# Kernel tuning notes

Hardware: AMD Instinct MI355X
Metric: run time of the kernel (lower is better)

Reference implementation:

```python
import jax, jax.numpy as jnp
import numpy as np

B, S, D, H = 4, 2048, 1024, 16
DK = D // H
SCALE = 1.0 / np.float32(np.sqrt(DK))


def setup_inputs() -> dict:
    key = jax.random.key(0)
    ks = jax.random.split(key, 11)
    w = lambda k: (jax.random.normal(k, (D, D), jnp.float32) * 0.02)
    b = lambda k: (jax.random.normal(k, (D,), jnp.float32) * 0.02)
    return {
        "Q": jax.random.normal(ks[0], (B, S, D), jnp.float32),
        "K": jax.random.normal(ks[1], (B, S, D), jnp.float32),
        "V": jax.random.normal(ks[2], (B, S, D), jnp.float32),
        "Wq": w(ks[3]), "bq": b(ks[4]),
        "Wk": w(ks[5]), "bk": b(ks[6]),
        "Wv": w(ks[7]), "bv": b(ks[8]),
        "Wo": w(ks[9]), "bo": b(ks[10]),
        # causal mask, broadcast over batch and heads: [1,1,S,S]
        "mask": jnp.tril(jnp.ones((1, 1, S, S), dtype=bool)),
    }


def reference(Q, K, V, Wq, bq, Wk, bk, Wv, bv, Wo, bo, mask):
    def proj(x, W, bias):
        # [B,S,D] -> [B,H,S,DK]
        return (x @ W + bias).reshape(B, S, H, DK).transpose(0, 2, 1, 3)

    q = proj(Q, Wq, bq)
    k = proj(K, Wk, bk)
    v = proj(V, Wv, bv)
    scores = jnp.einsum("bhqd,bhkd->bhqk", q, k) * SCALE  # [B,H,S,S]
    scores = jnp.where(mask, scores, jnp.float32(-1e9))
    attn = jax.nn.softmax(scores, axis=-1)
    out = jnp.einsum("bhqk,bhkd->bhqd", attn, v)  # [B,H,S,DK]
    out = out.transpose(0, 2, 1, 3).reshape(B, S, D)
    return out @ Wo + bo
```

## Files before the change

### kernel.cpp

```cpp
#include <hip/hip_runtime.h>
#include <hip/hip_bf16.h>
#include <stdint.h>

#define BB 4
#define SS 2048
#define DD 1024
#define HH 16
#define DKK 64
#define MM (BB * SS)

typedef __hip_bfloat16 bf16;
typedef __attribute__((ext_vector_type(8))) short frag8;
typedef __attribute__((ext_vector_type(4))) float f32x4;

#define GLDS16(g, l)                                                        \
  __builtin_amdgcn_global_load_lds(                                         \
      (const __attribute__((address_space(1))) void*)(g),                   \
      (__attribute__((address_space(3))) void*)(l), 16, 0, 0)

#define MFMA __builtin_amdgcn_mfma_f32_16x16x32_bf16
#define SBAR asm volatile("s_barrier" ::: "memory")
#define WAITV0 asm volatile("s_waitcnt vmcnt(0)" ::: "memory")

__device__ __forceinline__ unsigned short f2bu(float f) {
  __hip_bfloat16 h = __float2bfloat16(f);
  return *reinterpret_cast<unsigned short*>(&h);
}

struct WtArgs {
  const float* s[3];
  unsigned short* d[3];
};
__global__ __launch_bounds__(256) void wtrans_kernel(WtArgs a) {
  const float* __restrict__ W = a.s[blockIdx.z];
  unsigned short* __restrict__ Wt = a.d[blockIdx.z];
  __shared__ float t[64][68];
  const int n0 = blockIdx.x * 64, k0 = blockIdx.y * 64;
  const int tid = threadIdx.x;
#pragma unroll
  for (int it = 0; it < 4; ++it) {
    const int kk = it * 16 + (tid >> 4);
    const int nn = (tid & 15) * 4;
    const float4 v = *(const float4*)&W[(size_t)(k0 + kk) * DD + n0 + nn];
    *(float4*)&t[kk][nn] = v;
  }
  __syncthreads();
#pragma unroll
  for (int it = 0; it < 2; ++it) {
    const int n = it * 32 + (tid >> 3);
    const int c = tid & 7;
    frag8 pk;
#pragma unroll
    for (int j = 0; j < 8; ++j) pk[j] = (short)f2bu(t[c * 8 + j][n]);
    *(frag8*)&Wt[(size_t)(n0 + n) * DD + k0 + c * 8] = pk;
  }
}

struct CvtArgs {
  const float* s[3];
  unsigned short* d[3];
};
__global__ __launch_bounds__(256) void cvt_kernel(CvtArgs a) {
  const float* __restrict__ src = a.s[blockIdx.y];
  unsigned short* __restrict__ dst = a.d[blockIdx.y];
  const size_t i = ((size_t)blockIdx.x * 256 + threadIdx.x) * 8;
  const float4 v0 = *(const float4*)&src[i];
  const float4 v1 = *(const float4*)&src[i + 4];
  frag8 pk;
  pk[0] = (short)f2bu(v0.x); pk[1] = (short)f2bu(v0.y);
  pk[2] = (short)f2bu(v0.z); pk[3] = (short)f2bu(v0.w);
  pk[4] = (short)f2bu(v1.x); pk[5] = (short)f2bu(v1.y);
  pk[6] = (short)f2bu(v1.z); pk[7] = (short)f2bu(v1.w);
  *(frag8*)&dst[i] = pk;
}

struct GArgs {
  const void* A[3];
  const unsigned short* W[3];
  const float* bias[3];
  void* out[3];
  float oscale[3];
  int abf16[3];
  int omode[3];
};

__global__ __launch_bounds__(512, 2) void gemm8_kernel(GArgs ga) {
  constexpr int K = DD;
  const int nwg = gridDim.x;
  const int q = nwg >> 3;
  const int o = blockIdx.x;
  const int wgid = (o & 7) * q + (o >> 3);
  const int z = wgid >> 7;
  const int rem = wgid & 127;
  const int mt = rem >> 2, nt = rem & 3;
  const int m0 = mt * 256, n0 = nt * 256;

  const unsigned short* __restrict__ A = (const unsigned short*)ga.A[z];
  const unsigned short* __restrict__ Wt = ga.W[z];
  const float* __restrict__ bias = ga.bias[z];
  void* __restrict__ outv = ga.out[z];
  const float oscale = ga.oscale[z];
  const int omode = ga.omode[z];

  __shared__ unsigned short As[2][256 * 64];
  __shared__ unsigned short Bs[2][256 * 64];

  const int tid = threadIdx.x;
  const int wave = tid >> 6, lane = tid & 63, quad = lane >> 4, l15 = lane & 15;
  const int wr = wave >> 2, wc = wave & 3;

  f32x4 acc[8][4] = {};
  frag8 af[4][2], bfv[2][2];

  auto stage4 = [&](int b, int k0, int half) {
#pragma unroll
    for (int ii = 0; ii < 4; ++ii) {
      const int i = half * 4 + ii;
      const int g = i * 8 + wave;
      const int rs = (g & 31) * 8;
      const int lrow = rs + (lane >> 3);
      const int gc = ((lane & 7) ^ (lane >> 3)) * 8;
      const unsigned off = __builtin_amdgcn_readfirstlane(
          (unsigned)(b * 32768 + rs * 128));
      if (g < 32) {
        GLDS16(&A[(size_t)(m0 + lrow) * K + k0 + gc], (char*)&As[0][0] + off);
      } else {
        GLDS16(&Wt[(size_t)(n0 + lrow) * K + k0 + gc], (char*)&Bs[0][0] + off);
      }
    }
  };
  auto rdA = [&](int bt, int mh) {
#pragma unroll
    for (int mi = 0; mi < 4; ++mi)
#pragma unroll
      for (int s = 0; s < 2; ++s)
        af[mi][s] = *(const frag8*)&As[bt][(wr * 128 + mh * 64 + mi * 16 + l15) *
                                              64 +
                                          (((s * 4 + quad) ^ (l15 & 7)) * 8)];
  };
  auto rdB = [&](int bt, int nh) {
#pragma unroll
    for (int ni = 0; ni < 2; ++ni)
#pragma unroll
      for (int s = 0; s < 2; ++s)
        bfv[ni][s] = *(const frag8*)&Bs[bt][(wc * 64 + nh * 32 + ni * 16 + l15) *
                                                64 +
                                            (((s * 4 + quad) ^ (l15 & 7)) * 8)];
  };
  auto mma = [&](int mh, int nh) {
    __builtin_amdgcn_s_setprio(1);
#pragma unroll
    for (int s = 0; s < 2; ++s)
#pragma unroll
      for (int mi = 0; mi < 4; ++mi)
#pragma unroll
        for (int ni = 0; ni < 2; ++ni)
          acc[mh * 4 + mi][nh * 2 + ni] = MFMA(
              af[mi][s], bfv[ni][s], acc[mh * 4 + mi][nh * 2 + ni], 0, 0, 0);
    __builtin_amdgcn_s_setprio(0);
  };

  stage4(0, 0, 0);
  stage4(0, 0, 1);
  WAITV0;
  __syncthreads();

#pragma unroll 1
  for (int t = 0; t < 16; ++t) {
    const int bt = t & 1;
    const int nb = bt ^ 1;
    const bool pf = (t + 1 < 16);
    const int k1 = (t + 1) * 64;
    if (pf) stage4(nb, k1, 0);
    rdA(bt, 0);
    rdB(bt, 0);
    SBAR;
    mma(0, 0);
    SBAR;
    if (pf) stage4(nb, k1, 1);
    rdB(bt, 1);
    SBAR;
    mma(0, 1);
    SBAR;
    rdA(bt, 1);
    rdB(bt, 0);
    SBAR;
    mma(1, 0);
    SBAR;
    rdB(bt, 1);
    SBAR;
    mma(1, 1);
    WAITV0;
    SBAR;
  }

#pragma unroll
  for (int mi = 0; mi < 8; ++mi) {
#pragma unroll
    for (int ni = 0; ni < 4; ++ni) {
#pragma unroll
      for (int r = 0; r < 4; ++r) {
        const int grow = m0 + wr * 128 + mi * 16 + quad * 4 + r;
        const int gcol = n0 + wc * 64 + ni * 16 + l15;
        const float val = (acc[mi][ni][r] + bias[gcol]) * oscale;
        if (omode == 2) {
          ((float*)outv)[(size_t)grow * DD + gcol] = val;
        } else {
          const int b = grow / SS, s = grow % SS;
          const int h = gcol / DKK, dk = gcol % DKK;
          unsigned short* outp = (unsigned short*)outv;
          if (omode == 0)
            outp[(((size_t)(b * HH + h)) * SS + s) * DKK + dk] = f2bu(val);
          else
            outp[(((size_t)(b * HH + h)) * DKK + dk) * SS + s] = f2bu(val);
        }
      }
    }
  }
}

__global__ __launch_bounds__(256) void gemm_kernel(GArgs ga) {
  constexpr int K = DD;
  const int z = blockIdx.z;
  const void* __restrict__ Av = ga.A[z];
  const unsigned short* __restrict__ Wt = ga.W[z];
  const float* __restrict__ bias = ga.bias[z];
  void* __restrict__ outv = ga.out[z];
  const float oscale = ga.oscale[z];
  const int abf = ga.abf16[z];
  const int omode = ga.omode[z];

  __shared__ unsigned short Bs[2][128 * 64];
  __shared__ unsigned short As[2][128 * 64];
  const int tid = threadIdx.x;
  const int wave = tid >> 6, lane = tid & 63, quad = lane >> 4, l15 = lane & 15;
  const int wr = wave >> 1, wc = wave & 1;
  const int mt = blockIdx.x * 8 + (blockIdx.y >> 3);
  const int nt = blockIdx.y & 7;
  const int m0 = mt * 128, n0 = nt * 128;

  f32x4 acc[4][4] = {};
  float4 r0[4], r1[4];

  auto stageB = [&](int buf, int k0) {
#pragma unroll
    for (int c = 0; c < 4; ++c) {
      const int row = c * 32 + wave * 8 + (lane >> 3);
      const int gc = ((lane & 7) ^ (row & 7)) * 8;
      const unsigned short* g = &Wt[(size_t)(n0 + row) * K + k0 + gc];
      unsigned off = __builtin_amdgcn_readfirstlane(
          (unsigned)(buf * 16384 + (c * 32 + wave * 8) * 128));
      GLDS16(g, (char*)&Bs[0][0] + off);
    }
  };
  auto stageA16 = [&](int buf, int k0) {
    const unsigned short* Ap = (const unsigned short*)Av;
#pragma unroll
    for (int c = 0; c < 4; ++c) {
      const int row = c * 32 + wave * 8 + (lane >> 3);
      const int gc = ((lane & 7) ^ (row & 7)) * 8;
      const unsigned short* g = &Ap[(size_t)(m0 + row) * K + k0 + gc];
      unsigned off = __builtin_amdgcn_readfirstlane(
          (unsigned)(buf * 16384 + (c * 32 + wave * 8) * 128));
      GLDS16(g, (char*)&As[0][0] + off);
    }
  };
  auto loadA32 = [&](int k0) {
    const float* Ap = (const float*)Av;
#pragma unroll
    for (int it = 0; it < 4; ++it) {
      const int row = it * 32 + (tid >> 3);
      const int c = tid & 7;
      r0[it] = *(const float4*)&Ap[(size_t)(m0 + row) * K + k0 + c * 8];
      r1[it] = *(const float4*)&Ap[(size_t)(m0 + row) * K + k0 + c * 8 + 4];
    }
  };
  auto writeA32 = [&](int buf) {
#pragma unroll
    for (int it = 0; it < 4; ++it) {
      const int row = it * 32 + (tid >> 3);
      const int c = tid & 7;
      frag8 pk;
      pk[0] = (short)f2bu(r0[it].x); pk[1] = (short)f2bu(r0[it].y);
      pk[2] = (short)f2bu(r0[it].z); pk[3] = (short)f2bu(r0[it].w);
      pk[4] = (short)f2bu(r1[it].x); pk[5] = (short)f2bu(r1[it].y);
      pk[6] = (short)f2bu(r1[it].z); pk[7] = (short)f2bu(r1[it].w);
      *(frag8*)&As[buf][row * 64 + ((c ^ (row & 7)) * 8)] = pk;
    }
  };
  auto compute = [&](int buf) {
#pragma unroll
    for (int s = 0; s < 2; ++s) {
      frag8 a2[4], b2[4];
#pragma unroll
      for (int mi = 0; mi < 4; ++mi)
        a2[mi] = *(const frag8*)&As[buf][(wr * 64 + mi * 16 + l15) * 64 +
                                         (((s * 4 + quad) ^ (l15 & 7)) * 8)];
#pragma unroll
      for (int ni = 0; ni < 4; ++ni)
        b2[ni] = *(const frag8*)&Bs[buf][(wc * 64 + ni * 16 + l15) * 64 +
                                         (((s * 4 + quad) ^ (l15 & 7)) * 8)];
#pragma unroll
      for (int mi = 0; mi < 4; ++mi)
#pragma unroll
        for (int ni = 0; ni < 4; ++ni)
          acc[mi][ni] = MFMA(a2[mi], b2[ni], acc[mi][ni], 0, 0, 0);
    }
  };

  if (abf) {
    stageB(0, 0);
    stageA16(0, 0);
  } else {
    loadA32(0);
    stageB(0, 0);
    writeA32(0);
  }
  __syncthreads();

#pragma unroll 1
  for (int t = 0; t < 16; t += 2) {
    if (t + 1 < 16) {
      if (abf) {
        stageB(1, (t + 1) * 64);
        stageA16(1, (t + 1) * 64);
      } else {
        loadA32((t + 1) * 64);
        stageB(1, (t + 1) * 64);
      }
    }
    compute(0);
    if (!abf && t + 1 < 16) writeA32(1);
    __syncthreads();
    if (t + 2 < 16) {
      if (abf) {
        stageB(0, (t + 2) * 64);
        stageA16(0, (t + 2) * 64);
      } else {
        loadA32((t + 2) * 64);
        stageB(0, (t + 2) * 64);
      }
    }
    compute(1);
    if (!abf && t + 2 < 16) writeA32(0);
    __syncthreads();
  }

#pragma unroll
  for (int mi = 0; mi < 4; ++mi) {
#pragma unroll
    for (int ni = 0; ni < 4; ++ni) {
#pragma unroll
      for (int r = 0; r < 4; ++r) {
        const int grow = m0 + wr * 64 + mi * 16 + quad * 4 + r;
        const int gcol = n0 + wc * 64 + ni * 16 + l15;
        const float val = (acc[mi][ni][r] + bias[gcol]) * oscale;
        if (omode == 2) {
          ((float*)outv)[(size_t)grow * DD + gcol] = val;
        } else {
          const int b = grow / SS, s = grow % SS;
          const int h = gcol / DKK, dk = gcol % DKK;
          unsigned short* outp = (unsigned short*)outv;
          if (omode == 0)
            outp[(((size_t)(b * HH + h)) * SS + s) * DKK + dk] = f2bu(val);
          else
            outp[(((size_t)(b * HH + h)) * DKK + dk) * SS + s] = f2bu(val);
        }
      }
    }
  }
}

__global__ __launch_bounds__(256) void fattn_kernel(
    const unsigned short* __restrict__ q, const unsigned short* __restrict__ k,
    const unsigned short* __restrict__ vt, unsigned short* __restrict__ ctx) {
  __shared__ unsigned short Ks[2][64 * 64];
  __shared__ unsigned short Vs[2][64 * 64];
  __shared__ unsigned short P_lds[4][16][36];
  const int tid = threadIdx.x;
  const int wave = tid >> 6, lane = tid & 63, quad = lane >> 4, l15 = lane & 15;
  const int bh = blockIdx.x & 63;
  const int tp = blockIdx.x >> 6;
  const size_t qkb = (size_t)bh * SS * DKK;
  const size_t vtb = (size_t)bh * DKK * SS;
  const int b = bh / HH, h = bh % HH;

  frag8 ones;
#pragma unroll
  for (int s = 0; s < 8; ++s) ones[s] = (short)0x3F80;

  auto stage = [&](int buf, int jt) {
#pragma unroll
    for (int c = 0; c < 2; ++c) {
      const int row = wave * 16 + c * 8 + (lane >> 3);
      const int gc = ((lane & 7) ^ (row & 7)) * 8;
      const unsigned short* g = &k[qkb + (size_t)(jt * 64 + row) * DKK + gc];
      unsigned off = __builtin_amdgcn_readfirstlane(
          (unsigned)(buf * 8192 + (wave * 16 + c * 8) * 128));
      GLDS16(g, (char*)&Ks[0][0] + off);
    }
#pragma unroll
    for (int c = 0; c < 2; ++c) {
      const int row = wave * 16 + c * 8 + (lane >> 3);
      const int gc = ((lane & 7) ^ (row & 7)) * 8;
      const unsigned short* g = &vt[vtb + (size_t)row * SS + jt * 64 + gc];
      unsigned off = __builtin_amdgcn_readfirstlane(
          (unsigned)(buf * 8192 + (wave * 16 + c * 8) * 128));
      GLDS16(g, (char*)&Vs[0][0] + off);
    }
  };

  for (int half = 0; half < 2; ++half) {
    const int t = half ? (31 - tp) : tp;
    const int q0 = t * 64 + wave * 16;

    const frag8 aq0 =
        *(const frag8*)&q[qkb + (size_t)(q0 + l15) * DKK + quad * 8];
    const frag8 aq1 =
        *(const frag8*)&q[qkb + (size_t)(q0 + l15) * DKK + 32 + quad * 8];

    f32x4 oacc[4] = {};
    f32x4 lacc = {};

    const int nT = t + 1;
    stage(0, 0);
    __syncthreads();

    for (int jt = 0; jt < nT; ++jt) {
      const int p = jt & 1;
      if (jt + 1 < nT) stage(1 - p, jt + 1);
      const bool diag = (jt == t);

#pragma unroll
      for (int jsub = 0; jsub < 2; ++jsub) {
        f32x4 sc[2];
#pragma unroll
        for (int g = 0; g < 2; ++g) {
          const int row = jsub * 32 + g * 16 + l15;
          const frag8 kf0 =
              *(const frag8*)&Ks[p][row * 64 + ((quad ^ (l15 & 7)) * 8)];
          const frag8 kf1 =
              *(const frag8*)&Ks[p][row * 64 + (((4 + quad) ^ (l15 & 7)) * 8)];
          f32x4 z = {};
          z = MFMA(aq0, kf0, z, 0, 0, 0);
          sc[g] = MFMA(aq1, kf1, z, 0, 0, 0);
        }
        float p0[4], p1[4];
        if (diag) {
          const int jg = jt * 64 + jsub * 32;
#pragma unroll
          for (int r = 0; r < 4; ++r) {
            const int ig = q0 + quad * 4 + r;
            p0[r] = (jg + l15 <= ig) ? __expf(sc[0][r]) : 0.f;
            p1[r] = (jg + 16 + l15 <= ig) ? __expf(sc[1][r]) : 0.f;
          }
        } else {
#pragma unroll
          for (int r = 0; r < 4; ++r) {
            p0[r] = __expf(sc[0][r]);
            p1[r] = __expf(sc[1][r]);
          }
        }
#pragma unroll
        for (int r = 0; r < 4; ++r) {
          P_lds[wave][quad * 4 + r][l15] = f2bu(p0[r]);
          P_lds[wave][quad * 4 + r][16 + l15] = f2bu(p1[r]);
        }
        const frag8 pa = *(const frag8*)&P_lds[wave][l15][quad * 8];
#pragma unroll
        for (int c = 0; c < 4; ++c) {
          const int vrow = c * 16 + l15;
          const int chunk = ((jsub * 4 + quad) ^ (l15 & 7));
          const frag8 vf = *(const frag8*)&Vs[p][vrow * 64 + chunk * 8];
          oacc[c] = MFMA(pa, vf, oacc[c], 0, 0, 0);
        }
        lacc = MFMA(pa, ones, lacc, 0, 0, 0);
      }
      __syncthreads();
    }

#pragma unroll
    for (int r = 0; r < 4; ++r) {
      const float inv = 1.f / lacc[r];
      const int ig = q0 + quad * 4 + r;
#pragma unroll
      for (int c = 0; c < 4; ++c)
        ctx[((size_t)(b * SS + ig)) * DD + h * DKK + c * 16 + l15] =
            f2bu(oacc[c][r] * inv);
    }
  }
}

extern "C" void kernel_launch(void* const* d_in, const int* in_sizes, int n_in,
                              void* d_out, int out_size, void* d_ws,
                              size_t ws_size, hipStream_t stream) {
  const float* Q = (const float*)d_in[0];
  const float* K = (const float*)d_in[1];
  const float* V = (const float*)d_in[2];
  const float* Wq = (const float*)d_in[3];
  const float* bq = (const float*)d_in[4];
  const float* Wk = (const float*)d_in[5];
  const float* bk = (const float*)d_in[6];
  const float* Wv = (const float*)d_in[7];
  const float* bv = (const float*)d_in[8];
  const float* Wo = (const float*)d_in[9];
  const float* bo = (const float*)d_in[10];

  const size_t NE = (size_t)MM * DD;
  unsigned short* ctx = (unsigned short*)d_ws;
  unsigned short* qp = ctx + NE;
  unsigned short* kp = qp + NE;
  unsigned short* vtp = kp + NE;
  unsigned short* Qb = vtp + NE;
  unsigned short* Kb = Qb + NE;
  unsigned short* Vb = Kb + NE;
  unsigned short* Wqt = ctx;
  unsigned short* Wkt = ctx + 1048576;
  unsigned short* Wvt = ctx + 2097152;
  unsigned short* Wot = qp;

  const bool fastQK = ws_size >= (size_t)6 * NE * sizeof(unsigned short);
  const bool fastV = ws_size >= (size_t)7 * NE * sizeof(unsigned short);

  WtArgs wa1;
  wa1.s[0] = Wq; wa1.s[1] = Wk; wa1.s[2] = Wv;
  wa1.d[0] = Wqt; wa1.d[1] = Wkt; wa1.d[2] = Wvt;
  wtrans_kernel<<<dim3(16, 16, 3), 256, 0, stream>>>(wa1);

  CvtArgs ca;
  if (fastQK) {
    int ncvt = 2;
    ca.s[0] = Q; ca.d[0] = Qb;
    ca.s[1] = K; ca.d[1] = Kb;
    if (fastV) { ca.s[2] = V; ca.d[2] = Vb; ncvt = 3; }
    cvt_kernel<<<dim3(NE / 2048, ncvt), 256, 0, stream>>>(ca);
  }

  GArgs g3;
  g3.A[0] = fastQK ? (const void*)Qb : (const void*)Q;
  g3.A[1] = fastQK ? (const void*)Kb : (const void*)K;
  g3.A[2] = fastV ? (const void*)Vb : (const void*)V;
  g3.W[0] = Wqt; g3.W[1] = Wkt; g3.W[2] = Wvt;
  g3.bias[0] = bq; g3.bias[1] = bk; g3.bias[2] = bv;
  g3.out[0] = qp; g3.out[1] = kp; g3.out[2] = vtp;
  g3.oscale[0] = 0.125f; g3.oscale[1] = 1.f; g3.oscale[2] = 1.f;
  g3.abf16[0] = fastQK ? 1 : 0; g3.abf16[1] = fastQK ? 1 : 0;
  g3.abf16[2] = fastV ? 1 : 0;
  g3.omode[0] = 0; g3.omode[1] = 0; g3.omode[2] = 1;
  if (fastV) {
    gemm8_kernel<<<dim3(384), 512, 0, stream>>>(g3);
  } else {
    gemm_kernel<<<dim3(8, 64, 3), 256, 0, stream>>>(g3);
  }

  fattn_kernel<<<dim3(BB * HH * 16), 256, 0, stream>>>(qp, kp, vtp, ctx);

  WtArgs wa2;
  wa2.s[0] = Wo; wa2.d[0] = Wot;
  wa2.s[1] = Wo; wa2.d[1] = Wot;
  wa2.s[2] = Wo; wa2.d[2] = Wot;
  wtrans_kernel<<<dim3(16, 16, 1), 256, 0, stream>>>(wa2);

  GArgs go;
  go.A[0] = (const void*)ctx; go.W[0] = Wot; go.bias[0] = bo;
  go.out[0] = (void*)d_out; go.oscale[0] = 1.f;
  go.abf16[0] = 1; go.omode[0] = 2;
  go.A[1] = go.A[0]; go.W[1] = go.W[0]; go.bias[1] = go.bias[0];
  go.out[1] = go.out[0]; go.oscale[1] = 1.f; go.abf16[1] = 1; go.omode[1] = 2;
  go.A[2] = go.A[0]; go.W[2] = go.W[0]; go.bias[2] = go.bias[0];
  go.out[2] = go.out[0]; go.oscale[2] = 1.f; go.abf16[2] = 1; go.omode[2] = 2;
  if (fastV) {
    gemm8_kernel<<<dim3(128), 512, 0, stream>>>(go);
  } else {
    gemm_kernel<<<dim3(8, 64, 1), 256, 0, stream>>>(go);
  }
}
```

Baseline: 433.0 us.

## Split GEMM prefetch into four units with partial vmcnt waits

Reorganizes the global-to-LDS prefetch of the projection GEMM into four units ordered to match the consumption order of the four MFMA sub-phases. Each phase waits only for the loads it needs via partial vmcnt counts, instead of draining all loads at the end of each k-iteration. This lets loads overlap compute across phases, so less time is spent stalled on memory. The cost is more fragile synchronization: the vmcnt counts and the unit-to-row mapping must exactly match the order in which data is consumed.

```diff
diff --git a/kernel.cpp b/kernel.cpp
--- a/kernel.cpp
+++ b/kernel.cpp
@@ -20,7 +20,7 @@
 
 #define MFMA __builtin_amdgcn_mfma_f32_16x16x32_bf16
 #define SBAR asm volatile("s_barrier" ::: "memory")
-#define WAITV0 asm volatile("s_waitcnt vmcnt(0)" ::: "memory")
+#define WAITN(n) asm volatile("s_waitcnt vmcnt(" #n ")" ::: "memory")
 
 __device__ __forceinline__ unsigned short f2bu(float f) {
   __hip_bfloat16 h = __float2bfloat16(f);
@@ -112,17 +112,22 @@
   f32x4 acc[8][4] = {};
   frag8 af[4][2], bfv[2][2];
 
-  auto stage4 = [&](int b, int k0, int half) {
-#pragma unroll
-    for (int ii = 0; ii < 4; ++ii) {
-      const int i = half * 4 + ii;
-      const int g = i * 8 + wave;
-      const int rs = (g & 31) * 8;
+  auto stageU = [&](int b, int k0, int unit) {
+#pragma unroll
+    for (int jj = 0; jj < 2; ++jj) {
+      const int j = wave + jj * 8;
+      int g;
+      bool isA;
+      if (unit == 0) { g = (j & 7) | ((j >> 3) << 4); isA = true; }
+      else if (unit == 1) { g = (j & 3) | ((j >> 2) << 3); isA = false; }
+      else if (unit == 2) { g = 4 + ((j & 3) | ((j >> 2) << 3)); isA = false; }
+      else { g = 8 + ((j & 7) | ((j >> 3) << 4)); isA = true; }
+      const int rs = g * 8;
       const int lrow = rs + (lane >> 3);
       const int gc = ((lane & 7) ^ (lane >> 3)) * 8;
       const unsigned off = __builtin_amdgcn_readfirstlane(
           (unsigned)(b * 32768 + rs * 128));
-      if (g < 32) {
+      if (isA) {
         GLDS16(&A[(size_t)(m0 + lrow) * K + k0 + gc], (char*)&As[0][0] + off);
       } else {
         GLDS16(&Wt[(size_t)(n0 + lrow) * K + k0 + gc], (char*)&Bs[0][0] + off);
@@ -160,9 +165,11 @@
     __builtin_amdgcn_s_setprio(0);
   };
 
-  stage4(0, 0, 0);
-  stage4(0, 0, 1);
-  WAITV0;
+  stageU(0, 0, 0);
+  stageU(0, 0, 1);
+  stageU(0, 0, 2);
+  stageU(0, 0, 3);
+  WAITN(4);
   __syncthreads();
 
 #pragma unroll 1
@@ -171,26 +178,30 @@
     const int nb = bt ^ 1;
     const bool pf = (t + 1 < 16);
     const int k1 = (t + 1) * 64;
-    if (pf) stage4(nb, k1, 0);
+    if (pf) stageU(nb, k1, 0);
     rdA(bt, 0);
     rdB(bt, 0);
+    if (pf) { WAITN(4); } else { WAITN(2); }
     SBAR;
     mma(0, 0);
     SBAR;
-    if (pf) stage4(nb, k1, 1);
+    if (pf) stageU(nb, k1, 1);
     rdB(bt, 1);
+    if (pf) { WAITN(4); } else { WAITN(0); }
     SBAR;
     mma(0, 1);
     SBAR;
+    if (pf) stageU(nb, k1, 2);
     rdA(bt, 1);
     rdB(bt, 0);
     SBAR;
     mma(1, 0);
     SBAR;
+    if (pf) stageU(nb, k1, 3);
     rdB(bt, 1);
+    if (pf) { WAITN(4); }
     SBAR;
     mma(1, 1);
-    WAITV0;
     SBAR;
   }
 
```

New measurement: 440.6 us. No clear change (+1.7%).
